# Kernel tuning notes

Hardware: AMD Instinct MI355X
Metric: run time of the kernel (lower is better)

Reference implementation:

```python
import jax, jax.numpy as jnp
import numpy as np

DIM = 1024
HEADS = 16
HEAD_DIM = DIM // HEADS  # 64


def get_rope_matrix(seq_len: int, dim: int) -> jnp.ndarray:
    # rope[s, d] = concat(cos(s * inv_freq), sin(s * inv_freq))  -> (seq_len, dim)
    half = dim // 2
    inv_freq = 1.0 / (10000.0 ** (jnp.arange(half, dtype=jnp.float32) / half))
    sinusoid = jnp.arange(seq_len, dtype=jnp.float32)[:, None] * inv_freq[None, :]
    return jnp.concatenate([jnp.cos(sinusoid), jnp.sin(sinusoid)], axis=-1)


def setup_inputs() -> dict:
    key = jax.random.key(0)
    ks = jax.random.split(key, 6)
    B, T, D = 2, 2048, DIM
    scale = 1.0 / np.sqrt(D)
    return {
        "x": jax.random.normal(ks[0], (B, T, D), dtype=jnp.float32),
        "Wq": jax.random.normal(ks[1], (D, D), dtype=jnp.float32) * scale,
        "Wk": jax.random.normal(ks[2], (D, D), dtype=jnp.float32) * scale,
        "Wv": jax.random.normal(ks[3], (D, D), dtype=jnp.float32) * scale,
        "Wo": jax.random.normal(ks[4], (D, D), dtype=jnp.float32) * scale,
        "bo": jax.random.normal(ks[5], (D,), dtype=jnp.float32) * 0.01,
    }


def reference(x, Wq, Wk, Wv, Wo, bo):
    B, T, D = x.shape
    H, hd = HEADS, HEAD_DIM

    # projections -> (B, H, T, hd)
    def split_heads(y):
        return y.reshape(B, T, H, hd).transpose(0, 2, 1, 3)

    q = split_heads(x @ Wq)
    k = split_heads(x @ Wk)
    v = split_heads(x @ Wv)

    rope = get_rope_matrix(T, hd)  # (T, hd)

    # apply_rope(v, rope): einsum('...nd,sd->...ns') contracts head_dim -> (B,H,T,T)
    v_r = jnp.einsum('bhnd,sd->bhns', v, rope)

    scores = jax.nn.softmax(jnp.einsum('bhnd,bhmd->bhnm', q, k) / jnp.sqrt(jnp.float32(hd)), axis=-1)
    out = jnp.einsum('bhnm,bhms->bhns', scores, v_r)  # (B,H,T,T)

    # apply_rope(out, rope.T): out2[...,n,s] = sum_t out[...,n,t] * rope[t,s] -> (B,H,T,hd)
    out = jnp.einsum('bhnt,ts->bhns', out, rope)

    out = out.transpose(0, 2, 1, 3).reshape(B, T, D)
    return out @ Wo + bo
```

## Files before the change

kernel.cpp:

```cpp
#include <hip/hip_runtime.h>
#include <math.h>

#define DIM 1024
#define NH 16
#define HD 64
#define TT 2048
#define NTOK 4096

typedef __bf16 bf8v __attribute__((ext_vector_type(8)));
typedef float f4v __attribute__((ext_vector_type(4)));
typedef unsigned short us8 __attribute__((ext_vector_type(8)));
typedef unsigned short us4 __attribute__((ext_vector_type(4)));

static __device__ __forceinline__ unsigned short f2bf(float f) {
    unsigned int u = __float_as_uint(f);
    u += 0x7FFFu + ((u >> 16) & 1u);
    return (unsigned short)(u >> 16);
}
static __device__ __forceinline__ bf8v ld8(const unsigned short* p) {
    return __builtin_bit_cast(bf8v, *(const us8*)p);
}
static __device__ __forceinline__ void gl_lds(const unsigned short* g, unsigned short* l) {
    __builtin_amdgcn_global_load_lds((const __attribute__((address_space(1))) unsigned int*)(g),
                                     (__attribute__((address_space(3))) unsigned int*)(l), 16, 0, 0);
}

__global__ void k_prep(const float* __restrict__ x, unsigned short* __restrict__ xb,
                       const float* __restrict__ Wq, const float* __restrict__ Wk,
                       const float* __restrict__ Wv, unsigned short* __restrict__ wt,
                       float* __restrict__ rope) {
    int tid = threadIdx.x;
    int bb = blockIdx.x;
    if (bb < 4096) {
        int i = bb * 256 + tid;
        float4 v = ((const float4*)x)[i];
        us4 o;
        o[0] = f2bf(v.x); o[1] = f2bf(v.y); o[2] = f2bf(v.z); o[3] = f2bf(v.w);
        *(us4*)&xb[i * 4] = o;
    } else if (bb < 7168) {
        __shared__ float tile[32][33];
        bb -= 4096;
        int z = bb >> 10, rem = bb & 1023;
        int bx = rem & 31, by = rem >> 5;
        const float* W = (z == 0) ? Wq : ((z == 1) ? Wk : Wv);
        int tx = tid & 31, ty = tid >> 5;
        int c0 = bx * 32, k0 = by * 32;
#pragma unroll
        for (int j = 0; j < 4; j++)
            tile[ty + j * 8][tx] = W[(k0 + ty + j * 8) * DIM + c0 + tx];
        __syncthreads();
        unsigned short* out = wt + z * DIM * DIM;
#pragma unroll
        for (int j = 0; j < 4; j++)
            out[(c0 + ty + j * 8) * DIM + k0 + tx] = f2bf(tile[tx][ty + j * 8]);
    } else {
        int i = (bb - 7168) * 256 + tid;
        int s = i >> 6, d = i & 63;
        float inv = exp2f(-(float)(d & 31) * (13.287712379549449f / 32.0f));
        float a = (float)s * inv;
        rope[i] = (d < 32) ? cosf(a) : sinf(a);
    }
}

__global__ void k_R(const float* __restrict__ rope, float* __restrict__ R) {
    __shared__ float red[256];
    int d = blockIdx.x;
    int e = threadIdx.x & 63, sl = threadIdx.x >> 6;
    const float* rp = rope + sl * 512 * 64;
    float acc = 0.f;
    for (int s = 0; s < 512; s++)
        acc += rp[s * 64 + d] * rp[s * 64 + e];
    red[threadIdx.x] = acc;
    __syncthreads();
    if (sl == 0)
        R[d * 64 + e] = (red[e] + red[e + 64]) + (red[e + 128] + red[e + 192]);
}

__global__ void k_wo2(const float* __restrict__ Wo, const float* __restrict__ R,
                      unsigned short* __restrict__ wo2t) {
    __shared__ float Ws[64 * 65];
    __shared__ float Rt[64 * 65];
    int tid = threadIdx.x;
    int h = blockIdx.y, j0 = blockIdx.x * 64;
    for (int idx = tid; idx < 4096; idx += 256) {
        int e = idx >> 6, j = idx & 63;
        Ws[e * 65 + j] = Wo[(h * 64 + e) * DIM + j0 + j];
        Rt[e * 65 + j] = R[j * 64 + e];
    }
    __syncthreads();
    int d = tid & 63, jb = (tid >> 6) * 16;
    float acc[16] = {};
    for (int e = 0; e < 64; e++) {
        float r = Rt[e * 65 + d];
#pragma unroll
        for (int jj = 0; jj < 16; jj++)
            acc[jj] += r * Ws[e * 65 + jb + jj];
    }
#pragma unroll
    for (int jj = 0; jj < 16; jj++)
        wo2t[(j0 + jb + jj) * DIM + h * 64 + d] = f2bf(acc[jj]);
}


__global__ __launch_bounds__(256, 3) void k_gemm_qkv(const unsigned short* __restrict__ A,
                                                     const unsigned short* __restrict__ Bt,
                                                     unsigned short* __restrict__ qk,
                                                     unsigned short* __restrict__ vt) {
    __shared__ unsigned short As[128 * 32];
    __shared__ unsigned short Bs[128 * 32];
    const int K = 1024;
    int tid = threadIdx.x;
    int lane = tid & 63, w = tid >> 6;
    int quad = lane >> 4, l16 = lane & 15;
    int m0 = blockIdx.y * 128, n0 = blockIdx.x * 128;
    int wm = (w >> 1) * 64, wn = (w & 1) * 64;

    int s0 = tid, s1 = 256 + tid;
    int r0 = s0 >> 2, cc0 = ((s0 & 3) ^ (r0 & 3)) * 8;
    int r1 = s1 >> 2, cc1 = ((s1 & 3) ^ (r1 & 3)) * 8;
    const unsigned short* Ag0 = A + (m0 + r0) * K + cc0;
    const unsigned short* Ag1 = A + (m0 + r1) * K + cc1;
    const unsigned short* Bg0 = Bt + (n0 + r0) * K + cc0;
    const unsigned short* Bg1 = Bt + (n0 + r1) * K + cc1;
    int qx = quad ^ (l16 & 3);

    f4v acc[4][4] = {};
    for (int k0 = 0; k0 < K; k0 += 32) {
        __syncthreads();
        gl_lds(Ag0 + k0, &As[s0 * 8]);
        gl_lds(Ag1 + k0, &As[s1 * 8]);
        gl_lds(Bg0 + k0, &Bs[s0 * 8]);
        gl_lds(Bg1 + k0, &Bs[s1 * 8]);
        __syncthreads();
        bf8v af[4], bf[4];
#pragma unroll
        for (int mt = 0; mt < 4; mt++)
            af[mt] = ld8(&As[(wm + mt * 16 + l16) * 32 + qx * 8]);
#pragma unroll
        for (int nt = 0; nt < 4; nt++)
            bf[nt] = ld8(&Bs[(wn + nt * 16 + l16) * 32 + qx * 8]);
#pragma unroll
        for (int mt = 0; mt < 4; mt++)
#pragma unroll
            for (int nt = 0; nt < 4; nt++)
                acc[mt][nt] = __builtin_amdgcn_mfma_f32_16x16x32_bf16(af[mt], bf[nt], acc[mt][nt], 0, 0, 0);
    }
#pragma unroll
    for (int mt = 0; mt < 4; mt++) {
#pragma unroll
        for (int nt = 0; nt < 4; nt++) {
            int gc = n0 + wn + nt * 16 + l16;
            int h = (gc >> 6) & 15;
            int d = gc & 63;
            if (gc < 2048) {
                float qs = (gc < 1024) ? 0.18033688011111793f : 1.0f;
                int mtx = gc >> 10;
                unsigned short* base = qk + mtx * (NTOK * DIM);
#pragma unroll
                for (int r = 0; r < 4; r++) {
                    int gm = m0 + wm + mt * 16 + quad * 4 + r;
                    int b = gm >> 11, t = gm & 2047;
                    base[((b * NH + h) * TT + t) * HD + d] = f2bf(acc[mt][nt][r] * qs);
                }
            } else {
                int gm0 = m0 + wm + mt * 16 + quad * 4;
                int b = gm0 >> 11, t = gm0 & 2047;
                us4 ov;
#pragma unroll
                for (int r = 0; r < 4; r++)
                    ov[r] = f2bf(acc[mt][nt][r]);
                *(us4*)&vt[(((b * NH + h) * HD) + d) * TT + t] = ov;
            }
        }
    }
}

__global__ __launch_bounds__(256, 3) void k_gemm_out(const unsigned short* __restrict__ A,
                                                     const unsigned short* __restrict__ Bt,
                                                     const float* __restrict__ bo,
                                                     float* __restrict__ out) {
    __shared__ unsigned short As[128 * 32];
    __shared__ unsigned short Bs[128 * 32];
    const int K = 1024;
    int tid = threadIdx.x;
    int lane = tid & 63, w = tid >> 6;
    int quad = lane >> 4, l16 = lane & 15;
    int m0 = blockIdx.y * 128, n0 = blockIdx.x * 128;
    int wm = (w >> 1) * 64, wn = (w & 1) * 64;

    int s0 = tid, s1 = 256 + tid;
    int r0 = s0 >> 2, cc0 = ((s0 & 3) ^ (r0 & 3)) * 8;
    int r1 = s1 >> 2, cc1 = ((s1 & 3) ^ (r1 & 3)) * 8;
    const unsigned short* Ag0 = A + (m0 + r0) * K + cc0;
    const unsigned short* Ag1 = A + (m0 + r1) * K + cc1;
    const unsigned short* Bg0 = Bt + (n0 + r0) * K + cc0;
    const unsigned short* Bg1 = Bt + (n0 + r1) * K + cc1;
    int qx = quad ^ (l16 & 3);

    f4v acc[4][4] = {};
    for (int k0 = 0; k0 < K; k0 += 32) {
        __syncthreads();
        gl_lds(Ag0 + k0, &As[s0 * 8]);
        gl_lds(Ag1 + k0, &As[s1 * 8]);
        gl_lds(Bg0 + k0, &Bs[s0 * 8]);
        gl_lds(Bg1 + k0, &Bs[s1 * 8]);
        __syncthreads();
        bf8v af[4], bf[4];
#pragma unroll
        for (int mt = 0; mt < 4; mt++)
            af[mt] = ld8(&As[(wm + mt * 16 + l16) * 32 + qx * 8]);
#pragma unroll
        for (int nt = 0; nt < 4; nt++)
            bf[nt] = ld8(&Bs[(wn + nt * 16 + l16) * 32 + qx * 8]);
#pragma unroll
        for (int mt = 0; mt < 4; mt++)
#pragma unroll
            for (int nt = 0; nt < 4; nt++)
                acc[mt][nt] = __builtin_amdgcn_mfma_f32_16x16x32_bf16(af[mt], bf[nt], acc[mt][nt], 0, 0, 0);
    }
#pragma unroll
    for (int mt = 0; mt < 4; mt++) {
#pragma unroll
        for (int nt = 0; nt < 4; nt++) {
            int gc = n0 + wn + nt * 16 + l16;
            float bias = bo[gc];
#pragma unroll
            for (int r = 0; r < 4; r++) {
                int gm = m0 + wm + mt * 16 + quad * 4 + r;
                out[gm * DIM + gc] = acc[mt][nt][r] + bias;
            }
        }
    }
}

#define LQ 72
__global__ __launch_bounds__(256, 4) void k_flash(const unsigned short* __restrict__ qk,
                                                  const unsigned short* __restrict__ vt,
                                                  unsigned short* __restrict__ Op,
                                                  float* __restrict__ Ls) {
    __shared__ unsigned short Ks[64 * LQ];
    __shared__ unsigned short Vs[80 * LQ];
    __shared__ unsigned short Ps[128 * LQ];
    int tid = threadIdx.x;
    int lane = tid & 63, w = tid >> 6;
    int quad = lane >> 4, l16 = lane & 15;
    int bh = blockIdx.x & 31;
    int sp = (blockIdx.x >> 5) & 1;
    int qt = blockIdx.x >> 6;
    const unsigned short* Qg = qk + bh * (TT * HD);
    const unsigned short* Kg = qk + NTOK * DIM + bh * (TT * HD);
    const unsigned short* Vtg = vt + bh * (HD * TT);

    for (int idx = tid; idx < 16 * LQ; idx += 256)
        Vs[64 * LQ + idx] = (idx < LQ) ? (unsigned short)0x3F80 : (unsigned short)0;

    {
        int r = tid >> 1, c0 = (tid & 1) * 32;
        const us8* src = (const us8*)(Qg + (qt * 128 + r) * HD + c0);
#pragma unroll
        for (int i = 0; i < 4; i++)
            *(us8*)&Ps[r * LQ + c0 + i * 8] = src[i];
    }
    bf8v qf[2][2];
#pragma unroll
    for (int g = 0; g < 2; g++)
#pragma unroll
        for (int ks = 0; ks < 2; ks++)
            qf[g][ks] = ld8(&Ps[(w * 32 + g * 16 + l16) * LQ + ks * 32 + quad * 8]);

    int sr = tid >> 2, sc = (tid & 3) * 16;
    const unsigned short* Kgp = Kg + (sp * 1024 + sr) * HD + sc;
    const unsigned short* Vgp = Vtg + sr * TT + sp * 1024 + sc;
    us8 kr0 = *(const us8*)(Kgp);
    us8 kr1 = *(const us8*)(Kgp + 8);
    us8 vr0 = *(const us8*)(Vgp);
    us8 vr1 = *(const us8*)(Vgp + 8);

    f4v oacc[5][2] = {};

    for (int it = 0; it < 16; it++) {
        __syncthreads();
        *(us8*)&Ks[sr * LQ + sc] = kr0;
        *(us8*)&Ks[sr * LQ + sc + 8] = kr1;
        *(us8*)&Vs[sr * LQ + sc] = vr0;
        *(us8*)&Vs[sr * LQ + sc + 8] = vr1;
        __syncthreads();
        if (it < 15) {
            Kgp += 64 * HD;
            Vgp += 64;
            kr0 = *(const us8*)(Kgp);
            kr1 = *(const us8*)(Kgp + 8);
            vr0 = *(const us8*)(Vgp);
            vr1 = *(const us8*)(Vgp + 8);
        }

        f4v sacc[4][2] = {};
#pragma unroll
        for (int ks = 0; ks < 2; ks++) {
            bf8v kf[4];
#pragma unroll
            for (int mt = 0; mt < 4; mt++)
                kf[mt] = ld8(&Ks[(mt * 16 + l16) * LQ + ks * 32 + quad * 8]);
#pragma unroll
            for (int mt = 0; mt < 4; mt++)
#pragma unroll
                for (int g = 0; g < 2; g++)
                    sacc[mt][g] = __builtin_amdgcn_mfma_f32_16x16x32_bf16(kf[mt], qf[g][ks], sacc[mt][g], 0, 0, 0);
        }

#pragma unroll
        for (int g = 0; g < 2; g++) {
#pragma unroll
            for (int mt = 0; mt < 4; mt++) {
                float p0 = __builtin_amdgcn_exp2f(sacc[mt][g][0]);
                float p1 = __builtin_amdgcn_exp2f(sacc[mt][g][1]);
                float p2 = __builtin_amdgcn_exp2f(sacc[mt][g][2]);
                float p3 = __builtin_amdgcn_exp2f(sacc[mt][g][3]);
                unsigned int d0 = __builtin_amdgcn_perm(__float_as_uint(p1), __float_as_uint(p0), 0x07060302u);
                unsigned int d1 = __builtin_amdgcn_perm(__float_as_uint(p3), __float_as_uint(p2), 0x07060302u);
                uint2 pk; pk.x = d0; pk.y = d1;
                *(uint2*)&Ps[(w * 32 + g * 16 + l16) * LQ + mt * 16 + quad * 4] = pk;
            }
        }

#pragma unroll
        for (int ks = 0; ks < 2; ks++) {
            bf8v pf[2];
#pragma unroll
            for (int g = 0; g < 2; g++)
                pf[g] = ld8(&Ps[(w * 32 + g * 16 + l16) * LQ + ks * 32 + quad * 8]);
#pragma unroll
            for (int mtd = 0; mtd < 5; mtd++) {
                bf8v vf = ld8(&Vs[(mtd * 16 + l16) * LQ + ks * 32 + quad * 8]);
#pragma unroll
                for (int g = 0; g < 2; g++)
                    oacc[mtd][g] = __builtin_amdgcn_mfma_f32_16x16x32_bf16(vf, pf[g], oacc[mtd][g], 0, 0, 0);
            }
        }
    }

    int b = bh >> 4, h = bh & 15;
    unsigned short* Opd = Op + sp * (NTOK * DIM);
#pragma unroll
    for (int g = 0; g < 2; g++) {
        int t = qt * 128 + w * 32 + g * 16 + l16;
        unsigned short* dst = Opd + (b * TT + t) * DIM + h * HD;
#pragma unroll
        for (int mtd = 0; mtd < 4; mtd++) {
            us4 ov;
#pragma unroll
            for (int r = 0; r < 4; r++)
                ov[r] = f2bf(oacc[mtd][g][r]);
            *(us4*)&dst[mtd * 16 + quad * 4] = ov;
        }
        if (quad == 0)
            Ls[sp * 65536 + bh * 2048 + t] = oacc[4][g][0];
    }
}

__global__ void k_comb(const unsigned short* __restrict__ Op, const float* __restrict__ Ls,
                       unsigned short* __restrict__ attn) {
    int e = (blockIdx.x * 256 + threadIdx.x) * 8;
    int h = (e >> 6) & 15, t = (e >> 10) & 2047, b = e >> 21;
    int bh = b * 16 + h;
    float inv = 1.0f / (Ls[bh * 2048 + t] + Ls[65536 + bh * 2048 + t]);
    us8 a = *(const us8*)&Op[e];
    us8 c = *(const us8*)&Op[NTOK * DIM + e];
    us8 o;
#pragma unroll
    for (int j = 0; j < 8; j++) {
        float fa = __uint_as_float((unsigned int)a[j] << 16);
        float fc = __uint_as_float((unsigned int)c[j] << 16);
        o[j] = f2bf((fa + fc) * inv);
    }
    *(us8*)&attn[e] = o;
}

extern "C" void kernel_launch(void* const* d_in, const int* in_sizes, int n_in,
                              void* d_out, int out_size, void* d_ws, size_t ws_size,
                              hipStream_t stream) {
    const float* x  = (const float*)d_in[0];
    const float* Wq = (const float*)d_in[1];
    const float* Wk = (const float*)d_in[2];
    const float* Wv = (const float*)d_in[3];
    const float* Wo = (const float*)d_in[4];
    const float* bo = (const float*)d_in[5];
    float* out = (float*)d_out;
    char* ws = (char*)d_ws;

    unsigned short* Xb    = (unsigned short*)(ws);
    unsigned short* Wqkvt = (unsigned short*)(ws + 8388608);
    unsigned short* Op    = (unsigned short*)(ws);
    unsigned short* QK    = (unsigned short*)(ws + 16777216);
    unsigned short* Vt    = (unsigned short*)(ws + 33554432);
    unsigned short* attn  = (unsigned short*)(ws + 41943040);
    unsigned short* Wo2t  = (unsigned short*)(ws + 50331648);
    float*          rope  = (float*)(ws + 52428800);
    float*          Rm    = (float*)(ws + 52953088);
    float*          Ls    = (float*)(ws + 52969472);

    hipLaunchKernelGGL(k_prep,     dim3(7680),   dim3(256), 0, stream, x, Xb, Wq, Wk, Wv, Wqkvt, rope);
    hipLaunchKernelGGL(k_R,        dim3(64),     dim3(256), 0, stream, rope, Rm);
    hipLaunchKernelGGL(k_wo2,      dim3(16, 16), dim3(256), 0, stream, Wo, Rm, Wo2t);
    hipLaunchKernelGGL(k_gemm_qkv, dim3(24, 32), dim3(256), 0, stream, Xb, Wqkvt, QK, Vt);
    hipLaunchKernelGGL(k_flash,    dim3(1024),   dim3(256), 0, stream, QK, Vt, Op, Ls);
    hipLaunchKernelGGL(k_comb,     dim3(2048),   dim3(256), 0, stream, Op, Ls, attn);
    hipLaunchKernelGGL(k_gemm_out, dim3(8, 32),  dim3(256), 0, stream, attn, Wo2t, bo, out);
}
```

Before: 220.4 us.

## Load K/V MFMA fragments directly from global memory, drop LDS staging and barriers

The flash kernel no longer stages K and V tiles through shared memory with double __syncthreads per iteration. Each wave now reads its MFMA fragments straight from global (L2/L1-cached) memory, and Q is also loaded directly. The row-sum tile that used to be an LDS row of ones is replaced by a register constant of bf16 ones. This removes barrier and LDS traffic and frees LDS for occupancy, but each wave now issues redundant uncoalesced global loads with no software prefetch, so latency may be exposed.

```diff
diff --git a/kernel.cpp b/kernel.cpp
--- a/kernel.cpp
+++ b/kernel.cpp
@@ -101,7 +101,6 @@
         wo2t[(j0 + jb + jj) * DIM + h * 64 + d] = f2bf(acc[jj]);
 }
 
-
 __global__ __launch_bounds__(256, 3) void k_gemm_qkv(const unsigned short* __restrict__ A,
                                                      const unsigned short* __restrict__ Bt,
                                                      unsigned short* __restrict__ qk,
@@ -238,8 +237,6 @@
                                                   const unsigned short* __restrict__ vt,
                                                   unsigned short* __restrict__ Op,
                                                   float* __restrict__ Ls) {
-    __shared__ unsigned short Ks[64 * LQ];
-    __shared__ unsigned short Vs[80 * LQ];
     __shared__ unsigned short Ps[128 * LQ];
     int tid = threadIdx.x;
     int lane = tid & 63, w = tid >> 6;
@@ -251,48 +248,25 @@
     const unsigned short* Kg = qk + NTOK * DIM + bh * (TT * HD);
     const unsigned short* Vtg = vt + bh * (HD * TT);
 
-    for (int idx = tid; idx < 16 * LQ; idx += 256)
-        Vs[64 * LQ + idx] = (idx < LQ) ? (unsigned short)0x3F80 : (unsigned short)0;
-
-    {
-        int r = tid >> 1, c0 = (tid & 1) * 32;
-        const us8* src = (const us8*)(Qg + (qt * 128 + r) * HD + c0);
-#pragma unroll
-        for (int i = 0; i < 4; i++)
-            *(us8*)&Ps[r * LQ + c0 + i * 8] = src[i];
-    }
     bf8v qf[2][2];
 #pragma unroll
     for (int g = 0; g < 2; g++)
 #pragma unroll
         for (int ks = 0; ks < 2; ks++)
-            qf[g][ks] = ld8(&Ps[(w * 32 + g * 16 + l16) * LQ + ks * 32 + quad * 8]);
-
-    int sr = tid >> 2, sc = (tid & 3) * 16;
-    const unsigned short* Kgp = Kg + (sp * 1024 + sr) * HD + sc;
-    const unsigned short* Vgp = Vtg + sr * TT + sp * 1024 + sc;
-    us8 kr0 = *(const us8*)(Kgp);
-    us8 kr1 = *(const us8*)(Kgp + 8);
-    us8 vr0 = *(const us8*)(Vgp);
-    us8 vr1 = *(const us8*)(Vgp + 8);
+            qf[g][ks] = ld8(Qg + (qt * 128 + w * 32 + g * 16 + l16) * HD + ks * 32 + quad * 8);
+
+    us8 one_u;
+#pragma unroll
+    for (int j = 0; j < 8; j++) one_u[j] = 0x3F80;
+    bf8v ones = __builtin_bit_cast(bf8v, one_u);
+
+    const unsigned short* Kb = Kg + (sp * 1024 + l16) * HD + quad * 8;
+    const unsigned short* Vb = Vtg + l16 * TT + sp * 1024 + quad * 8;
 
     f4v oacc[5][2] = {};
 
     for (int it = 0; it < 16; it++) {
-        __syncthreads();
-        *(us8*)&Ks[sr * LQ + sc] = kr0;
-        *(us8*)&Ks[sr * LQ + sc + 8] = kr1;
-        *(us8*)&Vs[sr * LQ + sc] = vr0;
-        *(us8*)&Vs[sr * LQ + sc + 8] = vr1;
-        __syncthreads();
-        if (it < 15) {
-            Kgp += 64 * HD;
-            Vgp += 64;
-            kr0 = *(const us8*)(Kgp);
-            kr1 = *(const us8*)(Kgp + 8);
-            vr0 = *(const us8*)(Vgp);
-            vr1 = *(const us8*)(Vgp + 8);
-        }
+        int key0 = it * 64;
 
         f4v sacc[4][2] = {};
 #pragma unroll
@@ -300,7 +274,7 @@
             bf8v kf[4];
 #pragma unroll
             for (int mt = 0; mt < 4; mt++)
-                kf[mt] = ld8(&Ks[(mt * 16 + l16) * LQ + ks * 32 + quad * 8]);
+                kf[mt] = ld8(Kb + (key0 + mt * 16) * HD + ks * 32);
 #pragma unroll
             for (int mt = 0; mt < 4; mt++)
 #pragma unroll
@@ -330,12 +304,15 @@
             for (int g = 0; g < 2; g++)
                 pf[g] = ld8(&Ps[(w * 32 + g * 16 + l16) * LQ + ks * 32 + quad * 8]);
 #pragma unroll
-            for (int mtd = 0; mtd < 5; mtd++) {
-                bf8v vf = ld8(&Vs[(mtd * 16 + l16) * LQ + ks * 32 + quad * 8]);
+            for (int mtd = 0; mtd < 4; mtd++) {
+                bf8v vf = ld8(Vb + mtd * 16 * TT + key0 + ks * 32);
 #pragma unroll
                 for (int g = 0; g < 2; g++)
                     oacc[mtd][g] = __builtin_amdgcn_mfma_f32_16x16x32_bf16(vf, pf[g], oacc[mtd][g], 0, 0, 0);
             }
+#pragma unroll
+            for (int g = 0; g < 2; g++)
+                oacc[4][g] = __builtin_amdgcn_mfma_f32_16x16x32_bf16(ones, pf[g], oacc[4][g], 0, 0, 0);
         }
     }
 
```

Result: slower. 296.7 us (+34.6%).

## Fuse split-combine into output GEMM and simplify flash row-sum and Q load

Applied to the files above, without the earlier changes.

Removes the separate k_comb kernel. The output GEMM now loads both split partial outputs and the row-sum normalizers itself, combining them in registers before writing the A tile to LDS, with the next tile prefetched in registers. In the flash kernel, Q fragments are loaded straight from global memory instead of being staged through LDS. The ones-row appended to the V tile in LDS is replaced by a register constant in a separate MFMA, which shrinks LDS use. This saves one launch and one bf16 round trip of the attention tensor, but the GEMM A path loses the async global_load_lds and now reads twice the bytes per tile with extra ALU work.

```diff
diff --git a/kernel.cpp b/kernel.cpp
--- a/kernel.cpp
+++ b/kernel.cpp
@@ -101,7 +101,6 @@
         wo2t[(j0 + jb + jj) * DIM + h * 64 + d] = f2bf(acc[jj]);
 }
 
-
 __global__ __launch_bounds__(256, 3) void k_gemm_qkv(const unsigned short* __restrict__ A,
                                                      const unsigned short* __restrict__ Bt,
                                                      unsigned short* __restrict__ qk,
@@ -175,7 +174,8 @@
     }
 }
 
-__global__ __launch_bounds__(256, 3) void k_gemm_out(const unsigned short* __restrict__ A,
+__global__ __launch_bounds__(256, 3) void k_gemm_out(const unsigned short* __restrict__ Op,
+                                                     const float* __restrict__ Ls,
                                                      const unsigned short* __restrict__ Bt,
                                                      const float* __restrict__ bo,
                                                      float* __restrict__ out) {
@@ -191,20 +191,48 @@
     int s0 = tid, s1 = 256 + tid;
     int r0 = s0 >> 2, cc0 = ((s0 & 3) ^ (r0 & 3)) * 8;
     int r1 = s1 >> 2, cc1 = ((s1 & 3) ^ (r1 & 3)) * 8;
-    const unsigned short* Ag0 = A + (m0 + r0) * K + cc0;
-    const unsigned short* Ag1 = A + (m0 + r1) * K + cc1;
+    int row0 = m0 + r0, row1 = m0 + r1;
+    const unsigned short* A0a = Op + row0 * K + cc0;
+    const unsigned short* A0b = Op + NTOK * DIM + row0 * K + cc0;
+    const unsigned short* A1a = Op + row1 * K + cc1;
+    const unsigned short* A1b = Op + NTOK * DIM + row1 * K + cc1;
+    int bt0 = (row0 >> 11) * 32768 + (row0 & 2047);
+    int bt1 = (row1 >> 11) * 32768 + (row1 & 2047);
     const unsigned short* Bg0 = Bt + (n0 + r0) * K + cc0;
     const unsigned short* Bg1 = Bt + (n0 + r1) * K + cc1;
     int qx = quad ^ (l16 & 3);
 
+    us8 pa0 = *(const us8*)(A0a), pb0 = *(const us8*)(A0b);
+    us8 pa1 = *(const us8*)(A1a), pb1 = *(const us8*)(A1b);
+    float pi0 = 1.0f / (Ls[bt0 + (cc0 >> 6) * 2048] + Ls[65536 + bt0 + (cc0 >> 6) * 2048]);
+    float pi1 = 1.0f / (Ls[bt1 + (cc1 >> 6) * 2048] + Ls[65536 + bt1 + (cc1 >> 6) * 2048]);
+
     f4v acc[4][4] = {};
     for (int k0 = 0; k0 < K; k0 += 32) {
         __syncthreads();
-        gl_lds(Ag0 + k0, &As[s0 * 8]);
-        gl_lds(Ag1 + k0, &As[s1 * 8]);
+        us8 o0, o1;
+#pragma unroll
+        for (int j = 0; j < 8; j++) {
+            float fa = __uint_as_float((unsigned int)pa0[j] << 16);
+            float fc = __uint_as_float((unsigned int)pb0[j] << 16);
+            o0[j] = f2bf((fa + fc) * pi0);
+            float ga = __uint_as_float((unsigned int)pa1[j] << 16);
+            float gc2 = __uint_as_float((unsigned int)pb1[j] << 16);
+            o1[j] = f2bf((ga + gc2) * pi1);
+        }
+        *(us8*)&As[s0 * 8] = o0;
+        *(us8*)&As[s1 * 8] = o1;
         gl_lds(Bg0 + k0, &Bs[s0 * 8]);
         gl_lds(Bg1 + k0, &Bs[s1 * 8]);
         __syncthreads();
+        if (k0 + 32 < K) {
+            int kn = k0 + 32;
+            pa0 = *(const us8*)(A0a + kn);  pb0 = *(const us8*)(A0b + kn);
+            pa1 = *(const us8*)(A1a + kn);  pb1 = *(const us8*)(A1b + kn);
+            int h0 = (kn + cc0) >> 6, h1 = (kn + cc1) >> 6;
+            pi0 = 1.0f / (Ls[bt0 + h0 * 2048] + Ls[65536 + bt0 + h0 * 2048]);
+            pi1 = 1.0f / (Ls[bt1 + h1 * 2048] + Ls[65536 + bt1 + h1 * 2048]);
+        }
         bf8v af[4], bf[4];
 #pragma unroll
         for (int mt = 0; mt < 4; mt++)
@@ -239,7 +267,7 @@
                                                   unsigned short* __restrict__ Op,
                                                   float* __restrict__ Ls) {
     __shared__ unsigned short Ks[64 * LQ];
-    __shared__ unsigned short Vs[80 * LQ];
+    __shared__ unsigned short Vs[64 * LQ];
     __shared__ unsigned short Ps[128 * LQ];
     int tid = threadIdx.x;
     int lane = tid & 63, w = tid >> 6;
@@ -251,22 +279,17 @@
     const unsigned short* Kg = qk + NTOK * DIM + bh * (TT * HD);
     const unsigned short* Vtg = vt + bh * (HD * TT);
 
-    for (int idx = tid; idx < 16 * LQ; idx += 256)
-        Vs[64 * LQ + idx] = (idx < LQ) ? (unsigned short)0x3F80 : (unsigned short)0;
-
-    {
-        int r = tid >> 1, c0 = (tid & 1) * 32;
-        const us8* src = (const us8*)(Qg + (qt * 128 + r) * HD + c0);
-#pragma unroll
-        for (int i = 0; i < 4; i++)
-            *(us8*)&Ps[r * LQ + c0 + i * 8] = src[i];
-    }
     bf8v qf[2][2];
 #pragma unroll
     for (int g = 0; g < 2; g++)
 #pragma unroll
         for (int ks = 0; ks < 2; ks++)
-            qf[g][ks] = ld8(&Ps[(w * 32 + g * 16 + l16) * LQ + ks * 32 + quad * 8]);
+            qf[g][ks] = ld8(Qg + (qt * 128 + w * 32 + g * 16 + l16) * HD + ks * 32 + quad * 8);
+
+    us8 one_u;
+#pragma unroll
+    for (int j = 0; j < 8; j++) one_u[j] = 0x3F80;
+    bf8v ones = __builtin_bit_cast(bf8v, one_u);
 
     int sr = tid >> 2, sc = (tid & 3) * 16;
     const unsigned short* Kgp = Kg + (sp * 1024 + sr) * HD + sc;
@@ -330,12 +353,15 @@
             for (int g = 0; g < 2; g++)
                 pf[g] = ld8(&Ps[(w * 32 + g * 16 + l16) * LQ + ks * 32 + quad * 8]);
 #pragma unroll
-            for (int mtd = 0; mtd < 5; mtd++) {
+            for (int mtd = 0; mtd < 4; mtd++) {
                 bf8v vf = ld8(&Vs[(mtd * 16 + l16) * LQ + ks * 32 + quad * 8]);
 #pragma unroll
                 for (int g = 0; g < 2; g++)
                     oacc[mtd][g] = __builtin_amdgcn_mfma_f32_16x16x32_bf16(vf, pf[g], oacc[mtd][g], 0, 0, 0);
             }
+#pragma unroll
+            for (int g = 0; g < 2; g++)
+                oacc[4][g] = __builtin_amdgcn_mfma_f32_16x16x32_bf16(ones, pf[g], oacc[4][g], 0, 0, 0);
         }
     }
 
@@ -356,24 +382,6 @@
         if (quad == 0)
             Ls[sp * 65536 + bh * 2048 + t] = oacc[4][g][0];
     }
-}
-
-__global__ void k_comb(const unsigned short* __restrict__ Op, const float* __restrict__ Ls,
-                       unsigned short* __restrict__ attn) {
-    int e = (blockIdx.x * 256 + threadIdx.x) * 8;
-    int h = (e >> 6) & 15, t = (e >> 10) & 2047, b = e >> 21;
-    int bh = b * 16 + h;
-    float inv = 1.0f / (Ls[bh * 2048 + t] + Ls[65536 + bh * 2048 + t]);
-    us8 a = *(const us8*)&Op[e];
-    us8 c = *(const us8*)&Op[NTOK * DIM + e];
-    us8 o;
-#pragma unroll
-    for (int j = 0; j < 8; j++) {
-        float fa = __uint_as_float((unsigned int)a[j] << 16);
-        float fc = __uint_as_float((unsigned int)c[j] << 16);
-        o[j] = f2bf((fa + fc) * inv);
-    }
-    *(us8*)&attn[e] = o;
 }
 
 extern "C" void kernel_launch(void* const* d_in, const int* in_sizes, int n_in,
@@ -393,7 +401,6 @@
     unsigned short* Op    = (unsigned short*)(ws);
     unsigned short* QK    = (unsigned short*)(ws + 16777216);
     unsigned short* Vt    = (unsigned short*)(ws + 33554432);
-    unsigned short* attn  = (unsigned short*)(ws + 41943040);
     unsigned short* Wo2t  = (unsigned short*)(ws + 50331648);
     float*          rope  = (float*)(ws + 52428800);
     float*          Rm    = (float*)(ws + 52953088);
@@ -404,6 +411,5 @@
     hipLaunchKernelGGL(k_wo2,      dim3(16, 16), dim3(256), 0, stream, Wo, Rm, Wo2t);
     hipLaunchKernelGGL(k_gemm_qkv, dim3(24, 32), dim3(256), 0, stream, Xb, Wqkvt, QK, Vt);
     hipLaunchKernelGGL(k_flash,    dim3(1024),   dim3(256), 0, stream, QK, Vt, Op, Ls);
-    hipLaunchKernelGGL(k_comb,     dim3(2048),   dim3(256), 0, stream, Op, Ls, attn);
-    hipLaunchKernelGGL(k_gemm_out, dim3(8, 32),  dim3(256), 0, stream, attn, Wo2t, bo, out);
-}
+    hipLaunchKernelGGL(k_gemm_out, dim3(8, 32),  dim3(256), 0, stream, Op, Ls, Wo2t, bo, out);
+}
```

New measurement: 233.1 us. 5.7% more time.
